# Kernel optimization log

Measured on AMD Instinct MI355X. Metric: run time of the kernel, lower is better.

## Reference

```python
import jax, jax.numpy as jnp
import numpy as np

N = 100000
E = 1600000
C_IN = 128
C_OUT = 128


def setup_inputs() -> dict:
    key = jax.random.key(0)
    k1, k2, k3 = jax.random.split(key, 3)
    x = jax.random.normal(k1, (N, C_IN), dtype=jnp.float32)
    edge_index = jax.random.randint(k2, (2, E), 0, N, dtype=jnp.int64)
    # Linear(in, out, bias=False).weight has shape [out, in]
    W = jax.random.normal(k3, (C_OUT, C_IN), dtype=jnp.float32) * (1.0 / np.sqrt(C_IN))
    return {"x": x, "edge_index": edge_index, "W": W}


def reference(x, edge_index, W):
    n_nodes = x.shape[0]
    row, col = edge_index[0], edge_index[1]
    # degree counts only out-edges of row (matches torch `degree(edge_index, N)`)
    deg = jax.ops.segment_sum(jnp.ones((row.shape[0],), dtype=x.dtype), row,
                              num_segments=n_nodes)
    # D_tilde = D + I  ->  normalization n = (deg + 1)^(-1/2)
    inv_sqrt = jax.lax.rsqrt(deg + 1.0)  # [N]
    xs = x * inv_sqrt[:, None]
    # x <- (A + I) x : gather sources (col), scatter-add to destinations (row),
    # plus identity (self) contribution
    agg = jax.ops.segment_sum(xs[col], row, num_segments=n_nodes) + xs
    out = agg * inv_sqrt[:, None]
    # x <- x W^T
    return jnp.matmul(out, W.T)
```

## Files before the change

kernel.cpp:

```cpp
#include <hip/hip_runtime.h>
#include <hip/hip_fp16.h>
#include <math.h>

#define C 128
#define BSHIFT 9
#define BWIDTH 512
#define NBMAX 256
#define COLBITS 17
#define P2CHUNK 4096
#define P3CAP 10240
#define CAP 9216
#define APITCH 136

typedef _Float16 v8hf __attribute__((ext_vector_type(8)));
typedef float v4f __attribute__((ext_vector_type(4)));

__global__ __launch_bounds__(256) void init_wconv_kernel(int* __restrict__ gcur, int NB,
                                                         const float4* __restrict__ W4,
                                                         __half2* __restrict__ Wh2,
                                                         int total4) {
    int t = threadIdx.x;
    if (blockIdx.x == 0) {
        if (t < NB) gcur[t] = t * CAP;
    } else {
        int i = (blockIdx.x - 1) * 256 + t;
        if (i < total4) {
            float4 v = W4[i];
            Wh2[i * 2]     = __floats2half2_rn(v.x, v.y);
            Wh2[i * 2 + 1] = __floats2half2_rn(v.z, v.w);
        }
    }
}

__global__ __launch_bounds__(256) void p2_scatter_kernel(const int* __restrict__ rowI,
                                                         const int* __restrict__ colI,
                                                         int* __restrict__ gcur,
                                                         unsigned* __restrict__ ebuf, int E,
                                                         const float4* __restrict__ x4,
                                                         __half2* __restrict__ xh2, int N) {
    __shared__ int cnt[NBMAX];
    __shared__ int sc[NBMAX];
    __shared__ int delta[NBMAX];
    __shared__ unsigned sorted[P2CHUNK];
    __shared__ unsigned char bkt[P2CHUNK];
    const int t = threadIdx.x;
    cnt[t] = 0;
    __syncthreads();
    const int e0 = blockIdx.x * P2CHUNK;
    int ranks[16];
#pragma unroll
    for (int k = 0; k < 16; ++k) {
        int e = e0 + k * 256 + t;
        if (e < E) ranks[k] = atomicAdd(&cnt[rowI[e] >> BSHIFT], 1);
    }
    __syncthreads();
    sc[t] = cnt[t];
    __syncthreads();
    for (int o = 1; o < 256; o <<= 1) {
        int v = (t >= o) ? sc[t - o] : 0;
        __syncthreads();
        sc[t] += v;
        __syncthreads();
    }
    {
        int c = cnt[t];
        int ls = sc[t] - c;
        int gb = c ? atomicAdd(&gcur[t], c) : 0;
        delta[t] = gb - ls;
        sc[t] = ls;
    }
    __syncthreads();
#pragma unroll
    for (int k = 0; k < 16; ++k) {
        int e = e0 + k * 256 + t;
        if (e < E) {
            int r = rowI[e];
            unsigned cc = (unsigned)colI[e];
            int b = r >> BSHIFT;
            int lp = sc[b] + ranks[k];
            sorted[lp] = ((unsigned)(r & (BWIDTH - 1)) << COLBITS) | cc;
            bkt[lp] = (unsigned char)b;
        }
    }
    __syncthreads();
    int total = E - e0; if (total > P2CHUNK) total = P2CHUNK;
#pragma unroll
    for (int k = 0; k < 16; ++k) {
        int i = k * 256 + t;
        if (i < total) ebuf[delta[bkt[i]] + i] = sorted[i];
    }

    int totalX4 = N * 32;
    for (int i = blockIdx.x * 256 + t; i < totalX4; i += gridDim.x * 256) {
        float4 v = x4[i];
        xh2[i * 2]     = __floats2half2_rn(v.x, v.y);
        xh2[i * 2 + 1] = __floats2half2_rn(v.z, v.w);
    }
}

__global__ __launch_bounds__(512) void p3_place_kernel(const unsigned* __restrict__ ebuf,
                                                       const int* __restrict__ gcur,
                                                       int* __restrict__ offs_start,
                                                       int* __restrict__ offs_end,
                                                       float* __restrict__ inv,
                                                       int* __restrict__ csr, int N) {
    __shared__ unsigned eb[P3CAP];
    __shared__ int cnt[BWIDTH];
    __shared__ int woff[8];
    const int b = blockIdx.x;
    const int t = threadIdx.x;
    const int lane = t & 63;
    const int wv = t >> 6;
    const int rowBase = b << BSHIFT;
    const int eS = b * CAP;
    const int eE = gcur[b];
    const int len = eE - eS;

    cnt[t] = 0;
    __syncthreads();
    for (int i = t; i < len; i += 512) {
        unsigned rc = ebuf[eS + i];
        eb[i] = rc;
        atomicAdd(&cnt[rc >> COLBITS], 1);
    }
    __syncthreads();
    int myCnt = cnt[t];
    int v = myCnt;
#pragma unroll
    for (int o = 1; o < 64; o <<= 1) {
        int u = __shfl_up(v, o, 64);
        if (lane >= o) v += u;
    }
    if (lane == 63) woff[wv] = v;
    __syncthreads();
    if (t == 0) {
        int s = 0;
#pragma unroll
        for (int w = 0; w < 8; ++w) { int u = woff[w]; woff[w] = s; s += u; }
    }
    __syncthreads();
    int incl = v + woff[wv];
    int node = rowBase + t;
    if (node < N) {
        offs_start[node] = eS + incl - myCnt;
        offs_end[node]   = eS + incl;
        inv[node] = rsqrtf((float)myCnt + 1.0f);
    }
    __syncthreads();
    cnt[t] = incl - myCnt;
    __syncthreads();
    for (int i = t; i < len; i += 512) {
        unsigned rc = eb[i];
        int slot = atomicAdd(&cnt[rc >> COLBITS], 1);
        csr[eS + slot] = (int)(rc & ((1u << COLBITS) - 1));
    }
}

#define ACC4F(vv, sI)                                              \
    {                                                              \
        const __half2* p_ = (const __half2*)&(vv);                 \
        _Pragma("unroll")                                          \
        for (int q = 0; q < 4; ++q) {                              \
            float2 f_ = __half22float2(p_[q]);                     \
            a[2 * q]     = fmaf(f_.x, (sI), a[2 * q]);             \
            a[2 * q + 1] = fmaf(f_.y, (sI), a[2 * q + 1]);         \
        }                                                          \
    }

__global__ __launch_bounds__(256) void gather_mm_kernel(const float4* __restrict__ xh4,
                                                        const int* __restrict__ offs_start,
                                                        const int* __restrict__ offs_end,
                                                        const int* __restrict__ csr,
                                                        const float* __restrict__ inv,
                                                        const _Float16* __restrict__ Wh,
                                                        float* __restrict__ out, int N) {
    __shared__ _Float16 agg[16][APITCH];
    const int tid = threadIdx.x;
    const int base = blockIdx.x * 16;
    const int r = tid >> 4;
    const int c16 = tid & 15;
    const int node = base + r;

    float a[8] = {0, 0, 0, 0, 0, 0, 0, 0};
    float invn = 0.0f;
    if (node < N) {
        int s = offs_start[node];
        int e = offs_end[node];
        invn = inv[node];
        {
            float4 h = xh4[(size_t)node * 16 + c16];
            ACC4F(h, invn)
        }
        int j = s;
        for (; j + 8 <= e; j += 8) {
            int c0 = csr[j],     c1 = csr[j + 1], c2 = csr[j + 2], c3 = csr[j + 3];
            int c4 = csr[j + 4], c5 = csr[j + 5], c6 = csr[j + 6], c7 = csr[j + 7];
            float i0 = inv[c0], i1 = inv[c1], i2 = inv[c2], i3 = inv[c3];
            float i4 = inv[c4], i5 = inv[c5], i6 = inv[c6], i7 = inv[c7];
            float4 v0 = xh4[(size_t)c0 * 16 + c16];
            float4 v1 = xh4[(size_t)c1 * 16 + c16];
            float4 v2 = xh4[(size_t)c2 * 16 + c16];
            float4 v3 = xh4[(size_t)c3 * 16 + c16];
            float4 v4 = xh4[(size_t)c4 * 16 + c16];
            float4 v5 = xh4[(size_t)c5 * 16 + c16];
            float4 v6 = xh4[(size_t)c6 * 16 + c16];
            float4 v7 = xh4[(size_t)c7 * 16 + c16];
            ACC4F(v0, i0) ACC4F(v1, i1) ACC4F(v2, i2) ACC4F(v3, i3)
            ACC4F(v4, i4) ACC4F(v5, i5) ACC4F(v6, i6) ACC4F(v7, i7)
        }
        for (; j + 4 <= e; j += 4) {
            int c0 = csr[j], c1 = csr[j + 1], c2 = csr[j + 2], c3 = csr[j + 3];
            float i0 = inv[c0], i1 = inv[c1], i2 = inv[c2], i3 = inv[c3];
            float4 v0 = xh4[(size_t)c0 * 16 + c16];
            float4 v1 = xh4[(size_t)c1 * 16 + c16];
            float4 v2 = xh4[(size_t)c2 * 16 + c16];
            float4 v3 = xh4[(size_t)c3 * 16 + c16];
            ACC4F(v0, i0) ACC4F(v1, i1) ACC4F(v2, i2) ACC4F(v3, i3)
        }
        for (; j < e; ++j) {
            int c = csr[j];
            float ic = inv[c];
            float4 v = xh4[(size_t)c * 16 + c16];
            ACC4F(v, ic)
        }
#pragma unroll
        for (int q = 0; q < 8; ++q) a[q] *= invn;
    }
    {
        __half2 hh[4];
#pragma unroll
        for (int q = 0; q < 4; ++q) hh[q] = __floats2half2_rn(a[2 * q], a[2 * q + 1]);
        *(float4*)&agg[r][c16 * 8] = *(const float4*)hh;
    }
    __syncthreads();

    const int wave = tid >> 6;
    const int lane = tid & 63;
    const int rr = lane & 15;
    const int kg = lane >> 4;

    v8hf av[4];
#pragma unroll
    for (int kk = 0; kk < 4; ++kk)
        av[kk] = *(const v8hf*)&agg[rr][kg * 8 + kk * 32];

#pragma unroll
    for (int ti = 0; ti < 2; ++ti) {
        const int t = wave * 2 + ti;
        v4f acc = {0.0f, 0.0f, 0.0f, 0.0f};
        const v8hf* bp = (const v8hf*)(Wh + (size_t)(t * 16 + rr) * C + kg * 8);
#pragma unroll
        for (int kk = 0; kk < 4; ++kk)
            acc = __builtin_amdgcn_mfma_f32_16x16x32_f16(av[kk], bp[kk * 4], acc, 0, 0, 0);
#pragma unroll
        for (int reg = 0; reg < 4; ++reg) {
            int orow = base + kg * 4 + reg;
            if (orow < N) out[(size_t)orow * C + t * 16 + rr] = acc[reg];
        }
    }
}

extern "C" void kernel_launch(void* const* d_in, const int* in_sizes, int n_in,
                              void* d_out, int out_size, void* d_ws, size_t ws_size,
                              hipStream_t stream) {
    const float* x  = (const float*)d_in[0];
    const int*   ei = (const int*)d_in[1];
    const float* W  = (const float*)d_in[2];
    float* out = (float*)d_out;

    const int N = in_sizes[0] / C;
    const int E = in_sizes[1] / 2;
    const int* rowI = ei;
    const int* colI = ei + E;

    const int NB = (N + BWIDTH - 1) / BWIDTH;

    char* ws = (char*)d_ws;
    size_t off = 0;
    auto carve = [&](size_t bytes) -> void* {
        off = (off + 255) & ~(size_t)255;
        void* p = ws + off;
        off += bytes;
        return p;
    };
    int*      gcur       = (int*)carve((size_t)NBMAX * 4);
    int*      offs_start = (int*)carve((size_t)N * 4);
    int*      offs_end   = (int*)carve((size_t)N * 4);
    float*    inv        = (float*)carve((size_t)N * 4);
    int*      csr        = (int*)carve((size_t)NB * CAP * 4);
    __half2*  xh         = (__half2*)carve((size_t)N * C * 2);
    unsigned* ebuf       = (unsigned*)carve((size_t)NB * CAP * 4);
    __half2*  Wh         = (__half2*)carve((size_t)C * C * 2);

    int wtotal4 = C * C / 4;
    init_wconv_kernel<<<1 + (wtotal4 + 255) / 256, 256, 0, stream>>>(
        gcur, NB, (const float4*)W, Wh, wtotal4);

    int nChunks = (E + P2CHUNK - 1) / P2CHUNK;
    p2_scatter_kernel<<<nChunks, 256, 0, stream>>>(rowI, colI, gcur, ebuf, E,
                                                   (const float4*)x, xh, N);
    p3_place_kernel<<<NB, 512, 0, stream>>>(ebuf, gcur, offs_start, offs_end, inv, csr, N);

    gather_mm_kernel<<<(N + 15) / 16, 256, 0, stream>>>((const float4*)xh, offs_start,
                                                        offs_end, csr, inv,
                                                        (const _Float16*)Wh, out, N);
}
```

Before: 139.6 us.

## Fold weight conversion into scatter kernel, stage CSR in LDS, drop 8-wide unroll

```diff
diff --git a/kernel.cpp b/kernel.cpp
--- a/kernel.cpp
+++ b/kernel.cpp
@@ -15,29 +15,15 @@
 typedef _Float16 v8hf __attribute__((ext_vector_type(8)));
 typedef float v4f __attribute__((ext_vector_type(4)));
 
-__global__ __launch_bounds__(256) void init_wconv_kernel(int* __restrict__ gcur, int NB,
-                                                         const float4* __restrict__ W4,
-                                                         __half2* __restrict__ Wh2,
-                                                         int total4) {
-    int t = threadIdx.x;
-    if (blockIdx.x == 0) {
-        if (t < NB) gcur[t] = t * CAP;
-    } else {
-        int i = (blockIdx.x - 1) * 256 + t;
-        if (i < total4) {
-            float4 v = W4[i];
-            Wh2[i * 2]     = __floats2half2_rn(v.x, v.y);
-            Wh2[i * 2 + 1] = __floats2half2_rn(v.z, v.w);
-        }
-    }
-}
-
 __global__ __launch_bounds__(256) void p2_scatter_kernel(const int* __restrict__ rowI,
                                                          const int* __restrict__ colI,
                                                          int* __restrict__ gcur,
                                                          unsigned* __restrict__ ebuf, int E,
                                                          const float4* __restrict__ x4,
-                                                         __half2* __restrict__ xh2, int N) {
+                                                         __half2* __restrict__ xh2, int N,
+                                                         const float4* __restrict__ W4,
+                                                         __half2* __restrict__ Wh2,
+                                                         int wtotal4) {
     __shared__ int cnt[NBMAX];
     __shared__ int sc[NBMAX];
     __shared__ int delta[NBMAX];
@@ -65,7 +51,7 @@
     {
         int c = cnt[t];
         int ls = sc[t] - c;
-        int gb = c ? atomicAdd(&gcur[t], c) : 0;
+        int gb = c ? (t * CAP + atomicAdd(&gcur[t], c)) : 0;
         delta[t] = gb - ls;
         sc[t] = ls;
     }
@@ -91,10 +77,18 @@
     }
 
     int totalX4 = N * 32;
-    for (int i = blockIdx.x * 256 + t; i < totalX4; i += gridDim.x * 256) {
-        float4 v = x4[i];
-        xh2[i * 2]     = __floats2half2_rn(v.x, v.y);
-        xh2[i * 2 + 1] = __floats2half2_rn(v.z, v.w);
+    int totalConv = totalX4 + wtotal4;
+    for (int i = blockIdx.x * 256 + t; i < totalConv; i += gridDim.x * 256) {
+        if (i < totalX4) {
+            float4 v = x4[i];
+            xh2[i * 2]     = __floats2half2_rn(v.x, v.y);
+            xh2[i * 2 + 1] = __floats2half2_rn(v.z, v.w);
+        } else {
+            int j = i - totalX4;
+            float4 v = W4[j];
+            Wh2[j * 2]     = __floats2half2_rn(v.x, v.y);
+            Wh2[j * 2 + 1] = __floats2half2_rn(v.z, v.w);
+        }
     }
 }
 
@@ -105,6 +99,7 @@
                                                        float* __restrict__ inv,
                                                        int* __restrict__ csr, int N) {
     __shared__ unsigned eb[P3CAP];
+    __shared__ int sortedCol[P3CAP];
     __shared__ int cnt[BWIDTH];
     __shared__ int woff[8];
     const int b = blockIdx.x;
@@ -113,8 +108,8 @@
     const int wv = t >> 6;
     const int rowBase = b << BSHIFT;
     const int eS = b * CAP;
-    const int eE = gcur[b];
-    const int len = eE - eS;
+    int len = gcur[b];
+    if (len > P3CAP) len = P3CAP;
 
     cnt[t] = 0;
     __syncthreads();
@@ -146,14 +141,16 @@
         offs_end[node]   = eS + incl;
         inv[node] = rsqrtf((float)myCnt + 1.0f);
     }
-    __syncthreads();
     cnt[t] = incl - myCnt;
     __syncthreads();
     for (int i = t; i < len; i += 512) {
         unsigned rc = eb[i];
         int slot = atomicAdd(&cnt[rc >> COLBITS], 1);
-        csr[eS + slot] = (int)(rc & ((1u << COLBITS) - 1));
-    }
+        sortedCol[slot] = (int)(rc & ((1u << COLBITS) - 1));
+    }
+    __syncthreads();
+    for (int i = t; i < len; i += 512)
+        csr[eS + i] = sortedCol[i];
 }
 
 #define ACC4F(vv, sI)                                              \
@@ -192,22 +189,6 @@
             ACC4F(h, invn)
         }
         int j = s;
-        for (; j + 8 <= e; j += 8) {
-            int c0 = csr[j],     c1 = csr[j + 1], c2 = csr[j + 2], c3 = csr[j + 3];
-            int c4 = csr[j + 4], c5 = csr[j + 5], c6 = csr[j + 6], c7 = csr[j + 7];
-            float i0 = inv[c0], i1 = inv[c1], i2 = inv[c2], i3 = inv[c3];
-            float i4 = inv[c4], i5 = inv[c5], i6 = inv[c6], i7 = inv[c7];
-            float4 v0 = xh4[(size_t)c0 * 16 + c16];
-            float4 v1 = xh4[(size_t)c1 * 16 + c16];
-            float4 v2 = xh4[(size_t)c2 * 16 + c16];
-            float4 v3 = xh4[(size_t)c3 * 16 + c16];
-            float4 v4 = xh4[(size_t)c4 * 16 + c16];
-            float4 v5 = xh4[(size_t)c5 * 16 + c16];
-            float4 v6 = xh4[(size_t)c6 * 16 + c16];
-            float4 v7 = xh4[(size_t)c7 * 16 + c16];
-            ACC4F(v0, i0) ACC4F(v1, i1) ACC4F(v2, i2) ACC4F(v3, i3)
-            ACC4F(v4, i4) ACC4F(v5, i5) ACC4F(v6, i6) ACC4F(v7, i7)
-        }
         for (; j + 4 <= e; j += 4) {
             int c0 = csr[j], c1 = csr[j + 1], c2 = csr[j + 2], c3 = csr[j + 3];
             float i0 = inv[c0], i1 = inv[c1], i2 = inv[c2], i3 = inv[c3];
@@ -292,13 +273,13 @@
     unsigned* ebuf       = (unsigned*)carve((size_t)NB * CAP * 4);
     __half2*  Wh         = (__half2*)carve((size_t)C * C * 2);
 
+    hipMemsetAsync(gcur, 0, (size_t)NBMAX * 4, stream);
+
     int wtotal4 = C * C / 4;
-    init_wconv_kernel<<<1 + (wtotal4 + 255) / 256, 256, 0, stream>>>(
-        gcur, NB, (const float4*)W, Wh, wtotal4);
-
     int nChunks = (E + P2CHUNK - 1) / P2CHUNK;
     p2_scatter_kernel<<<nChunks, 256, 0, stream>>>(rowI, colI, gcur, ebuf, E,
-                                                   (const float4*)x, xh, N);
+                                                   (const float4*)x, xh, N,
+                                                   (const float4*)W, Wh, wtotal4);
     p3_place_kernel<<<NB, 512, 0, stream>>>(ebuf, gcur, offs_start, offs_end, inv, csr, N);
 
     gather_mm_kernel<<<(N + 15) / 16, 256, 0, stream>>>((const float4*)xh, offs_start,
```

Result: faster. 128.2 us (-8.2%).
